# Kernel optimization log

Hardware: AMD Instinct MI355X
Metric: run time of the kernel (lower is better)

The kernel has to match this reference:

```python
import jax, jax.numpy as jnp
import numpy as np

B, S, HQ, HKV, DH = 1, 2048, 32, 8, 128
DE = HQ * DH  # DEmbed = 4096
G = HQ // HKV  # GQA group size = 4


def apply_rope(x, cs):
    # x: [B, S, H, DH]; cs: [2, S, 1, DH//2] (broadcast over B via leading dims)
    d = x.shape[-1] // 2
    x1, x2 = x[..., :d], x[..., d:]
    y1 = x1 * cs[0] + x2 * cs[1]
    y2 = -x1 * cs[1] + x2 * cs[0]
    return jnp.concatenate([y1, y2], axis=-1)


def setup_inputs() -> dict:
    key = jax.random.key(0)
    ks = jax.random.split(key, 5)
    x = jax.random.normal(ks[0], (B, S, DE), dtype=jnp.float32)
    # Precomputed rotary tables, shaped [2, S, 1, DH//2] so they broadcast over [B,S,H,DH//2]
    half = DH // 2
    inv_freq = 1.0 / (10000.0 ** (np.arange(half, dtype=np.float64) / half))
    ang = np.arange(S, dtype=np.float64)[:, None] * inv_freq[None, :]
    cos_sin_RoPE = jnp.asarray(
        np.stack([np.cos(ang), np.sin(ang)])[:, :, None, :], dtype=jnp.float32
    )
    sc = DE ** -0.5
    wq = jax.random.normal(ks[1], (DE, HQ * DH), dtype=jnp.float32) * sc
    wk = jax.random.normal(ks[2], (DE, HKV * DH), dtype=jnp.float32) * sc
    wv = jax.random.normal(ks[3], (DE, HKV * DH), dtype=jnp.float32) * sc
    wo = jax.random.normal(ks[4], (DE, DE), dtype=jnp.float32) * sc
    return {"x": x, "cos_sin_RoPE": cos_sin_RoPE, "wq": wq, "wk": wk, "wv": wv, "wo": wo}


def reference(x, cos_sin_RoPE, wq, wk, wv, wo):
    b, s, _ = x.shape
    q = (x @ wq).reshape(b, s, HQ, DH)
    k = (x @ wk).reshape(b, s, HKV, DH)
    v = (x @ wv).reshape(b, s, HKV, DH)
    q = apply_rope(q, cos_sin_RoPE)
    k = apply_rope(k, cos_sin_RoPE)
    # GQA causal SDPA: group query heads per kv head
    q = q.transpose(0, 2, 1, 3).reshape(b, HKV, G, s, DH)  # [b,kv,g,s,d]
    k = k.transpose(0, 2, 1, 3)  # [b,kv,s,d]
    v = v.transpose(0, 2, 1, 3)  # [b,kv,s,d]
    scale = DH ** -0.5
    scores = jnp.einsum('bkgsd,bktd->bkgst', q, k) * scale  # [b,kv,g,s,s]
    mask = jnp.tril(jnp.ones((s, s), dtype=bool))
    scores = jnp.where(mask, scores, jnp.finfo(scores.dtype).min)
    p = jax.nn.softmax(scores, axis=-1)
    o = jnp.einsum('bkgst,bktd->bkgsd', p, v)  # [b,kv,g,s,d]
    o = o.transpose(0, 3, 1, 2, 4).reshape(b, s, HQ * DH)
    return o @ wo
```

## Files before the change

### kernel.cpp

```cpp
#include <hip/hip_runtime.h>
#include <hip/hip_bf16.h>
#include <cstdint>
#include <cstddef>

typedef __bf16 bf16x8 __attribute__((ext_vector_type(8)));
typedef float floatx4 __attribute__((ext_vector_type(4)));

#define MFMA(a, b, c) __builtin_amdgcn_mfma_f32_16x16x32_bf16((a), (b), (c), 0, 0, 0)

__device__ __forceinline__ unsigned short f2bf(float f) {
  unsigned u = __builtin_bit_cast(unsigned, f);
  u += 0x7fffu + ((u >> 16) & 1u);
  return (unsigned short)(u >> 16);
}
__device__ __forceinline__ float bf2f(unsigned short h) {
  unsigned u = ((unsigned)h) << 16;
  return __builtin_bit_cast(float, u);
}
__device__ __forceinline__ float fast_exp2(float x) {
#if __has_builtin(__builtin_amdgcn_exp2f)
  return __builtin_amdgcn_exp2f(x);
#else
  return exp2f(x);
#endif
}

__device__ __forceinline__ void gl2lds16(const unsigned short* g, unsigned short* l) {
  __builtin_amdgcn_global_load_lds(
      (const __attribute__((address_space(1))) unsigned int*)g,
      (__attribute__((address_space(3))) unsigned int*)l, 16, 0, 0);
}

__global__ void convert_f32_bf16(const float* __restrict__ src,
                                 unsigned short* __restrict__ dst, int n4) {
  int i = blockIdx.x * 256 + threadIdx.x;
  if (i >= n4) return;
  float4 f = ((const float4*)src)[i];
  ushort4 o;
  o.x = f2bf(f.x); o.y = f2bf(f.y); o.z = f2bf(f.z); o.w = f2bf(f.w);
  ((ushort4*)dst)[i] = o;
}

__global__ void transpose_f32_bf16(const float* __restrict__ src,
                                   unsigned short* __restrict__ dst, int K, int N) {
  __shared__ float tile[64 * 65];
  int tn = blockIdx.x * 64, tk = blockIdx.y * 64;
  int r = threadIdx.x >> 4;
  int c4 = (threadIdx.x & 15) * 4;
#pragma unroll
  for (int i = 0; i < 4; i++) {
    float4 f = *(const float4*)&src[(size_t)(tk + r + 16 * i) * N + tn + c4];
    float* tr = &tile[(r + 16 * i) * 65 + c4];
    tr[0] = f.x; tr[1] = f.y; tr[2] = f.z; tr[3] = f.w;
  }
  __syncthreads();
#pragma unroll
  for (int i = 0; i < 4; i++) {
    ushort4 o;
    o.x = f2bf(tile[(c4 + 0) * 65 + r + 16 * i]);
    o.y = f2bf(tile[(c4 + 1) * 65 + r + 16 * i]);
    o.z = f2bf(tile[(c4 + 2) * 65 + r + 16 * i]);
    o.w = f2bf(tile[(c4 + 3) * 65 + r + 16 * i]);
    *(ushort4*)&dst[(size_t)(tn + r + 16 * i) * K + tk + c4] = o;
  }
}

template <bool F32OUT>
__global__ __launch_bounds__(256) void gemm_bt(const unsigned short* __restrict__ A,
                        const unsigned short* __restrict__ Bt,
                        void* __restrict__ C, int M, int N, int K) {
  __shared__ alignas(16) unsigned short Alds[128 * 64];
  __shared__ alignas(16) unsigned short Blds[128 * 64];
  const int tid = threadIdx.x;
  const int w = tid >> 6, L = tid & 63;
  const int lr = L & 15, lg = L >> 4;
  const int bm = blockIdx.y * 128, bn = blockIdx.x * 128;
  const int wm = (w >> 1) * 64, wn = (w & 1) * 64;
  floatx4 acc[4][4] = {};

  const int srow = L >> 3;
  const int pcg = L & 7;
  const int scg = (pcg ^ srow) * 8;

  const unsigned short* Ag = &A[(size_t)(bm + w * 32 + srow) * K + scg];
  const unsigned short* Bg = &Bt[(size_t)(bn + w * 32 + srow) * K + scg];
  unsigned short* Al = &Alds[(w * 32 + srow) * 64 + pcg * 8];
  unsigned short* Bl = &Blds[(w * 32 + srow) * 64 + pcg * 8];

  for (int k0 = 0; k0 < K; k0 += 64) {
#pragma unroll
    for (int i = 0; i < 4; i++) {
      gl2lds16(Ag + (size_t)(i * 8) * K, Al + i * 8 * 64);
      gl2lds16(Bg + (size_t)(i * 8) * K, Bl + i * 8 * 64);
    }
    Ag += 64; Bg += 64;
    __syncthreads();

#pragma unroll
    for (int kk = 0; kk < 2; kk++) {
      const int ofs = ((kk * 4 + lg) ^ (lr & 7)) * 8;
      bf16x8 af[4], bfr[4];
#pragma unroll
      for (int i = 0; i < 4; i++) {
        af[i]  = *(const bf16x8*)&Alds[(wm + i * 16 + lr) * 64 + ofs];
        bfr[i] = *(const bf16x8*)&Blds[(wn + i * 16 + lr) * 64 + ofs];
      }
#pragma unroll
      for (int mi = 0; mi < 4; mi++)
#pragma unroll
        for (int ni = 0; ni < 4; ni++)
          acc[mi][ni] = MFMA(af[mi], bfr[ni], acc[mi][ni]);
    }
    __syncthreads();
  }

#pragma unroll
  for (int mi = 0; mi < 4; mi++) {
#pragma unroll
    for (int ni = 0; ni < 4; ni++) {
#pragma unroll
      for (int r = 0; r < 4; r++) {
        size_t row = bm + wm + mi * 16 + lg * 4 + r;
        size_t col = bn + wn + ni * 16 + lr;
        float v = acc[mi][ni][r];
        if constexpr (F32OUT) ((float*)C)[row * N + col] = v;
        else ((unsigned short*)C)[row * N + col] = f2bf(v);
      }
    }
  }
}

__global__ void rope_kernel(unsigned short* __restrict__ X, const float* __restrict__ cs,
                            int H, int rowStride, int colOff, float scale) {
  int idx = blockIdx.x * 256 + threadIdx.x;
  int d = idx & 63;
  int h = (idx >> 6) % H;
  int s = idx / (64 * H);
  size_t base = (size_t)s * rowStride + colOff + (size_t)h * 128;
  float x1 = bf2f(X[base + d]), x2 = bf2f(X[base + d + 64]);
  float c = cs[s * 64 + d];
  float sn = cs[2048 * 64 + s * 64 + d];
  float y1 = (x1 * c + x2 * sn) * scale;
  float y2 = (x2 * c - x1 * sn) * scale;
  X[base + d] = f2bf(y1);
  X[base + d + 64] = f2bf(y2);
}

__global__ void v_transpose(const unsigned short* __restrict__ QKV,
                            unsigned short* __restrict__ Vt) {
  __shared__ unsigned short tile[32][33];
  int h = blockIdx.z;
  int s0 = blockIdx.x * 32, d0 = blockIdx.y * 32;
  int c = threadIdx.x & 31, r0 = threadIdx.x >> 5;
#pragma unroll
  for (int i = 0; i < 32; i += 8)
    tile[r0 + i][c] = QKV[(size_t)(s0 + r0 + i) * 6144 + 5120 + h * 128 + d0 + c];
  __syncthreads();
#pragma unroll
  for (int i = 0; i < 32; i += 8)
    Vt[(size_t)(h * 128 + d0 + r0 + i) * 2048 + s0 + c] = tile[c][r0 + i];
}

__global__ __launch_bounds__(256) void flash_kernel(
    const unsigned short* __restrict__ QKV,
    const unsigned short* __restrict__ Vt,
    unsigned short* __restrict__ O) {
  constexpr int PSTR = 72;
  __shared__ alignas(16) unsigned short Klds[64 * 128];
  __shared__ alignas(16) unsigned short Vlds[128 * 64];
  __shared__ alignas(16) unsigned short Plds[4 * 32 * PSTR];
  const int tid = threadIdx.x, w = tid >> 6, L = tid & 63;
  const int lr = L & 15, lg = L >> 4;
  const int bid = blockIdx.x;
  const int hk = bid & 7;
  const int hp = (bid >> 3) & 1;
  const int qb = 31 - (bid >> 4);
  const int hq = hk * 4 + hp * 2 + (w & 1);
  const int qr0 = qb * 64 + (w >> 1) * 32;
  const unsigned short* Kg = QKV + 4096;

  const int k_row = tid >> 4, k_lcg = tid & 15;
  const unsigned short* KgT = &Kg[(size_t)k_row * 6144 + hk * 128 + ((k_lcg ^ (k_row & 15)) * 8)];
  unsigned short* KlT = &Klds[k_row * 128 + k_lcg * 8];
  const int v_row = tid >> 3, v_lcg = tid & 7;
  const unsigned short* VgT = &Vt[(size_t)(hk * 128 + v_row) * 2048 + ((v_lcg ^ (v_row & 7)) * 8)];
  unsigned short* VlT = &Vlds[v_row * 64 + v_lcg * 8];

  bf16x8 qf[2][4];
#pragma unroll
  for (int mi = 0; mi < 2; mi++)
#pragma unroll
    for (int c = 0; c < 4; c++)
      qf[mi][c] = *(const bf16x8*)&QKV[(size_t)(qr0 + mi * 16 + lr) * 6144 + hq * 128 + c * 32 + lg * 8];

  floatx4 oacc[2][8] = {};
  float l_lane[2][4] = {};
  unsigned short* pw = &Plds[w * 32 * PSTR];

  for (int t = 0; t <= qb; t++) {
    const int kv0 = t * 64;
    __syncthreads();
#pragma unroll
    for (int i = 0; i < 4; i++) {
      gl2lds16(KgT + (size_t)(kv0 + i * 16) * 6144, KlT + i * 16 * 128);
      gl2lds16(VgT + kv0 + (size_t)(i * 32) * 2048, VlT + i * 32 * 64);
    }
    __syncthreads();

#pragma unroll
    for (int nt = 0; nt < 4; nt++) {
      bf16x8 kf[4];
#pragma unroll
      for (int c = 0; c < 4; c++)
        kf[c] = *(const bf16x8*)&Klds[(nt * 16 + lr) * 128 + (((c * 4 + lg) ^ lr) * 8)];
      floatx4 sc[2];
#pragma unroll
      for (int mi = 0; mi < 2; mi++) {
        floatx4 a = {};
#pragma unroll
        for (int c = 0; c < 4; c++) a = MFMA(qf[mi][c], kf[c], a);
        sc[mi] = a;
      }
      if (t == qb) {
#pragma unroll
        for (int mi = 0; mi < 2; mi++)
#pragma unroll
          for (int r = 0; r < 4; r++)
            if (kv0 + nt * 16 + lr > qr0 + mi * 16 + lg * 4 + r) sc[mi][r] = -3e38f;
      }
#pragma unroll
      for (int mi = 0; mi < 2; mi++)
#pragma unroll
        for (int r = 0; r < 4; r++) {
          float p = fast_exp2(sc[mi][r]);
          l_lane[mi][r] += p;
          pw[(mi * 16 + lg * 4 + r) * PSTR + nt * 16 + lr] = f2bf(p);
        }
    }

    bf16x8 pf[2][2];
#pragma unroll
    for (int mi = 0; mi < 2; mi++)
#pragma unroll
      for (int c = 0; c < 2; c++)
        pf[mi][c] = *(const bf16x8*)&pw[(mi * 16 + lr) * PSTR + c * 32 + lg * 8];

#pragma unroll
    for (int n = 0; n < 8; n++) {
#pragma unroll
      for (int c = 0; c < 2; c++) {
        bf16x8 vf = *(const bf16x8*)&Vlds[(n * 16 + lr) * 64 + (((c * 4 + lg) ^ (lr & 7)) * 8)];
#pragma unroll
        for (int mi = 0; mi < 2; mi++) oacc[mi][n] = MFMA(pf[mi][c], vf, oacc[mi][n]);
      }
    }
  }

  float linv[2][4];
#pragma unroll
  for (int mi = 0; mi < 2; mi++)
#pragma unroll
    for (int r = 0; r < 4; r++) {
      float l = l_lane[mi][r];
      l += __shfl_xor(l, 1);
      l += __shfl_xor(l, 2);
      l += __shfl_xor(l, 4);
      l += __shfl_xor(l, 8);
      linv[mi][r] = 1.0f / l;
    }

#pragma unroll
  for (int mi = 0; mi < 2; mi++)
#pragma unroll
    for (int n = 0; n < 8; n++)
#pragma unroll
      for (int r = 0; r < 4; r++) {
        size_t row = qr0 + mi * 16 + lg * 4 + r;
        size_t col = (size_t)hq * 128 + n * 16 + lr;
        O[row * 4096 + col] = f2bf(oacc[mi][n][r] * linv[mi][r]);
      }
}

extern "C" void kernel_launch(void* const* d_in, const int* in_sizes, int n_in,
                              void* d_out, int out_size, void* d_ws, size_t ws_size,
                              hipStream_t stream) {
  const float* x  = (const float*)d_in[0];
  const float* cs = (const float*)d_in[1];
  const float* wq = (const float*)d_in[2];
  const float* wk = (const float*)d_in[3];
  const float* wv = (const float*)d_in[4];
  const float* wo = (const float*)d_in[5];
  float* out = (float*)d_out;

  char* ws = (char*)d_ws;
  unsigned short* xb   = (unsigned short*)(ws);
  unsigned short* wqt  = (unsigned short*)(ws + 16777216);
  unsigned short* wkt  = (unsigned short*)(ws + 50331648);
  unsigned short* wvt  = (unsigned short*)(ws + 58720256);
  unsigned short* wot  = (unsigned short*)(ws + 67108864);
  unsigned short* QKVb = (unsigned short*)(ws + 100663296);
  unsigned short* Vtb  = (unsigned short*)(ws + 125829120);
  unsigned short* Ob   = xb;

  convert_f32_bf16<<<8192, 256, 0, stream>>>(x, xb, 2097152);
  transpose_f32_bf16<<<dim3(64, 64), 256, 0, stream>>>(wq, wqt, 4096, 4096);
  transpose_f32_bf16<<<dim3(16, 64), 256, 0, stream>>>(wk, wkt, 4096, 1024);
  transpose_f32_bf16<<<dim3(16, 64), 256, 0, stream>>>(wv, wvt, 4096, 1024);
  transpose_f32_bf16<<<dim3(64, 64), 256, 0, stream>>>(wo, wot, 4096, 4096);

  gemm_bt<false><<<dim3(48, 16), 256, 0, stream>>>(xb, wqt, QKVb, 2048, 6144, 4096);

  rope_kernel<<<16384, 256, 0, stream>>>(QKVb, cs, 32, 6144, 0, 0.12751743f);
  rope_kernel<<<4096, 256, 0, stream>>>(QKVb, cs, 8, 6144, 4096, 1.0f);

  v_transpose<<<dim3(64, 4, 8), 256, 0, stream>>>(QKVb, Vtb);

  flash_kernel<<<512, 256, 0, stream>>>(QKVb, Vtb, Ob);

  gemm_bt<true><<<dim3(32, 16), 256, 0, stream>>>(Ob, wot, out, 2048, 4096, 4096);
}
```

Before: 501.5 us.

## Replace GEMM with double-buffered 512-thread pipelined kernel and vectorize RoPE

Replaces the single-buffered 128x128 GEMM with a 512-thread kernel using 256-wide N tiles (256x256 for QKV, 128x256 for output projection). It double-buffers LDS, interleaves global-to-LDS prefetches of tile T+2 between MFMA clusters, and uses explicit waitcnt, barriers and setprio to overlap memory with compute. RoPE is also vectorized to process four elements per thread with 64-bit loads and stores. The output-projection grid shrinks to 256 blocks, and the larger tiles raise register and LDS pressure, which could hurt occupancy or load balance.

```diff
diff --git a/kernel.cpp b/kernel.cpp
--- a/kernel.cpp
+++ b/kernel.cpp
@@ -7,6 +7,10 @@
 typedef float floatx4 __attribute__((ext_vector_type(4)));
 
 #define MFMA(a, b, c) __builtin_amdgcn_mfma_f32_16x16x32_bf16((a), (b), (c), 0, 0, 0)
+#define WAITVM(N) asm volatile("s_waitcnt vmcnt(" #N ")" ::: "memory")
+#define WAITLGKM0() asm volatile("s_waitcnt lgkmcnt(0)" ::: "memory")
+#define BARRIER() do { asm volatile("" ::: "memory"); __builtin_amdgcn_s_barrier(); asm volatile("" ::: "memory"); } while (0)
+#define SCHEDBAR() __builtin_amdgcn_sched_barrier(0)
 
 __device__ __forceinline__ unsigned short f2bf(float f) {
   unsigned u = __builtin_bit_cast(unsigned, f);
@@ -65,61 +69,128 @@
   }
 }
 
-template <bool F32OUT>
-__global__ __launch_bounds__(256) void gemm_bt(const unsigned short* __restrict__ A,
-                        const unsigned short* __restrict__ Bt,
-                        void* __restrict__ C, int M, int N, int K) {
-  __shared__ alignas(16) unsigned short Alds[128 * 64];
-  __shared__ alignas(16) unsigned short Blds[128 * 64];
+template <int MI, int MLO>
+__device__ __forceinline__ void mfma_cluster(floatx4 (&acc)[MI][4],
+                                             const bf16x8* a, const bf16x8* b) {
+  __builtin_amdgcn_s_setprio(1);
+#pragma unroll
+  for (int mi = 0; mi < 4; ++mi)
+#pragma unroll
+    for (int ni = 0; ni < 4; ++ni)
+      acc[MLO + mi][ni] = MFMA(a[MLO + mi], b[ni], acc[MLO + mi][ni]);
+  __builtin_amdgcn_s_setprio(0);
+}
+
+template <int MI, bool F32OUT>
+__global__ __launch_bounds__(512, 2) void gemm_pipe(
+    const unsigned short* __restrict__ A,
+    const unsigned short* __restrict__ Bt,
+    void* __restrict__ C, int M, int N, int K) {
+  constexpr int BM = MI * 32;
+  constexpr int NSA = BM / 64;
+  __shared__ alignas(16) unsigned short Al[2][BM * 64];
+  __shared__ alignas(16) unsigned short Bl[2][256 * 64];
   const int tid = threadIdx.x;
   const int w = tid >> 6, L = tid & 63;
   const int lr = L & 15, lg = L >> 4;
-  const int bm = blockIdx.y * 128, bn = blockIdx.x * 128;
-  const int wm = (w >> 1) * 64, wn = (w & 1) * 64;
-  floatx4 acc[4][4] = {};
-
-  const int srow = L >> 3;
-  const int pcg = L & 7;
-  const int scg = (pcg ^ srow) * 8;
-
-  const unsigned short* Ag = &A[(size_t)(bm + w * 32 + srow) * K + scg];
-  const unsigned short* Bg = &Bt[(size_t)(bn + w * 32 + srow) * K + scg];
-  unsigned short* Al = &Alds[(w * 32 + srow) * 64 + pcg * 8];
-  unsigned short* Bl = &Blds[(w * 32 + srow) * 64 + pcg * 8];
-
-  for (int k0 = 0; k0 < K; k0 += 64) {
-#pragma unroll
-    for (int i = 0; i < 4; i++) {
-      gl2lds16(Ag + (size_t)(i * 8) * K, Al + i * 8 * 64);
-      gl2lds16(Bg + (size_t)(i * 8) * K, Bl + i * 8 * 64);
-    }
-    Ag += 64; Bg += 64;
-    __syncthreads();
-
-#pragma unroll
-    for (int kk = 0; kk < 2; kk++) {
-      const int ofs = ((kk * 4 + lg) ^ (lr & 7)) * 8;
-      bf16x8 af[4], bfr[4];
-#pragma unroll
-      for (int i = 0; i < 4; i++) {
-        af[i]  = *(const bf16x8*)&Alds[(wm + i * 16 + lr) * 64 + ofs];
-        bfr[i] = *(const bf16x8*)&Blds[(wn + i * 16 + lr) * 64 + ofs];
-      }
-#pragma unroll
-      for (int mi = 0; mi < 4; mi++)
-#pragma unroll
-        for (int ni = 0; ni < 4; ni++)
-          acc[mi][ni] = MFMA(af[mi], bfr[ni], acc[mi][ni]);
-    }
-    __syncthreads();
-  }
-
-#pragma unroll
-  for (int mi = 0; mi < 4; mi++) {
-#pragma unroll
-    for (int ni = 0; ni < 4; ni++) {
-#pragma unroll
-      for (int r = 0; r < 4; r++) {
+  const int bm = blockIdx.y * BM, bn = blockIdx.x * 256;
+  const int wm = (w >> 2) * (MI * 16);
+  const int wn = (w & 3) * 64;
+  const int NT = K >> 6;
+
+  const int srow = tid >> 3, spcg = tid & 7;
+  const unsigned short* Ag = &A[(size_t)(bm + srow) * K + ((spcg ^ (srow & 7)) * 8)];
+  const unsigned short* Bg = &Bt[(size_t)(bn + srow) * K + ((spcg ^ (srow & 7)) * 8)];
+  unsigned short* AlT = &Al[0][0] + tid * 8;
+  unsigned short* BlT = &Bl[0][0] + tid * 8;
+
+#pragma unroll
+  for (int t = 0; t < 2; ++t) {
+#pragma unroll
+    for (int j = 0; j < NSA; ++j)
+      gl2lds16(Ag + (size_t)(j * 64) * K + t * 64, AlT + t * (BM * 64) + j * 4096);
+#pragma unroll
+    for (int j = 0; j < 4; ++j)
+      gl2lds16(Bg + (size_t)(j * 64) * K + t * 64, BlT + t * (256 * 64) + j * 4096);
+  }
+
+  floatx4 acc[MI][4] = {};
+
+  if constexpr (MI == 8) WAITVM(8); else WAITVM(6);
+  BARRIER();
+
+  for (int T = 0; T < NT; ++T) {
+    const int b = T & 1;
+    const unsigned short* Ab = &Al[b][0];
+    const unsigned short* Bb = &Bl[b][0];
+    bf16x8 a0[MI], a1[MI], b0[4], b1[4];
+#pragma unroll
+    for (int mi = 0; mi < MI; ++mi)
+      a0[mi] = *(const bf16x8*)&Ab[(wm + mi * 16 + lr) * 64 + ((lg ^ (lr & 7)) * 8)];
+#pragma unroll
+    for (int ni = 0; ni < 4; ++ni)
+      b0[ni] = *(const bf16x8*)&Bb[(wn + ni * 16 + lr) * 64 + ((lg ^ (lr & 7)) * 8)];
+#pragma unroll
+    for (int mi = 0; mi < MI; ++mi)
+      a1[mi] = *(const bf16x8*)&Ab[(wm + mi * 16 + lr) * 64 + (((4 + lg) ^ (lr & 7)) * 8)];
+#pragma unroll
+    for (int ni = 0; ni < 4; ++ni)
+      b1[ni] = *(const bf16x8*)&Bb[(wn + ni * 16 + lr) * 64 + (((4 + lg) ^ (lr & 7)) * 8)];
+
+    const bool st = (T + 2) < NT;
+    const size_t kofs = (size_t)(T + 2) * 64;
+    unsigned short* Ad = AlT + b * (BM * 64);
+    unsigned short* Bd = BlT + b * (256 * 64);
+
+    if constexpr (MI == 8) {
+      mfma_cluster<8, 0>(acc, a0, b0);
+      WAITLGKM0();
+      BARRIER(); SCHEDBAR();
+      if (st) {
+        gl2lds16(Ag + kofs, Ad);
+        gl2lds16(Ag + (size_t)64 * K + kofs, Ad + 4096);
+        gl2lds16(Ag + (size_t)128 * K + kofs, Ad + 8192);
+      }
+      mfma_cluster<8, 4>(acc, a0, b0);
+      BARRIER(); SCHEDBAR();
+      if (st) {
+        gl2lds16(Ag + (size_t)192 * K + kofs, Ad + 12288);
+        gl2lds16(Bg + kofs, Bd);
+        gl2lds16(Bg + (size_t)64 * K + kofs, Bd + 4096);
+      }
+      mfma_cluster<8, 0>(acc, a1, b1);
+      BARRIER(); SCHEDBAR();
+      if (st) {
+        gl2lds16(Bg + (size_t)128 * K + kofs, Bd + 8192);
+        gl2lds16(Bg + (size_t)192 * K + kofs, Bd + 12288);
+      }
+      mfma_cluster<8, 4>(acc, a1, b1);
+      if (st) { WAITVM(8); } else if (T + 1 < NT) { WAITVM(0); }
+      BARRIER(); SCHEDBAR();
+    } else {
+      mfma_cluster<4, 0>(acc, a0, b0);
+      WAITLGKM0();
+      BARRIER(); SCHEDBAR();
+      if (st) {
+        gl2lds16(Ag + kofs, Ad);
+        gl2lds16(Ag + (size_t)64 * K + kofs, Ad + 4096);
+        gl2lds16(Bg + kofs, Bd);
+        gl2lds16(Bg + (size_t)64 * K + kofs, Bd + 4096);
+        gl2lds16(Bg + (size_t)128 * K + kofs, Bd + 8192);
+        gl2lds16(Bg + (size_t)192 * K + kofs, Bd + 12288);
+      }
+      mfma_cluster<4, 0>(acc, a1, b1);
+      if (st) { WAITVM(6); } else if (T + 1 < NT) { WAITVM(0); }
+      BARRIER(); SCHEDBAR();
+    }
+  }
+
+#pragma unroll
+  for (int mi = 0; mi < MI; ++mi) {
+#pragma unroll
+    for (int ni = 0; ni < 4; ++ni) {
+#pragma unroll
+      for (int r = 0; r < 4; ++r) {
         size_t row = bm + wm + mi * 16 + lg * 4 + r;
         size_t col = bn + wn + ni * 16 + lr;
         float v = acc[mi][ni][r];
@@ -133,17 +204,37 @@
 __global__ void rope_kernel(unsigned short* __restrict__ X, const float* __restrict__ cs,
                             int H, int rowStride, int colOff, float scale) {
   int idx = blockIdx.x * 256 + threadIdx.x;
-  int d = idx & 63;
-  int h = (idx >> 6) % H;
-  int s = idx / (64 * H);
-  size_t base = (size_t)s * rowStride + colOff + (size_t)h * 128;
-  float x1 = bf2f(X[base + d]), x2 = bf2f(X[base + d + 64]);
-  float c = cs[s * 64 + d];
-  float sn = cs[2048 * 64 + s * 64 + d];
-  float y1 = (x1 * c + x2 * sn) * scale;
-  float y2 = (x2 * c - x1 * sn) * scale;
-  X[base + d] = f2bf(y1);
-  X[base + d + 64] = f2bf(y2);
+  int dg = idx & 15;
+  int h = (idx >> 4) % H;
+  int s = idx / (16 * H);
+  size_t base = (size_t)s * rowStride + colOff + (size_t)h * 128 + dg * 4;
+  ushort4 xa = *(const ushort4*)&X[base];
+  ushort4 xb = *(const ushort4*)&X[base + 64];
+  float4 c = *(const float4*)&cs[s * 64 + dg * 4];
+  float4 sn = *(const float4*)&cs[2048 * 64 + s * 64 + dg * 4];
+  ushort4 oa, ob;
+  {
+    float x1 = bf2f(xa.x), x2 = bf2f(xb.x);
+    oa.x = f2bf((x1 * c.x + x2 * sn.x) * scale);
+    ob.x = f2bf((x2 * c.x - x1 * sn.x) * scale);
+  }
+  {
+    float x1 = bf2f(xa.y), x2 = bf2f(xb.y);
+    oa.y = f2bf((x1 * c.y + x2 * sn.y) * scale);
+    ob.y = f2bf((x2 * c.y - x1 * sn.y) * scale);
+  }
+  {
+    float x1 = bf2f(xa.z), x2 = bf2f(xb.z);
+    oa.z = f2bf((x1 * c.z + x2 * sn.z) * scale);
+    ob.z = f2bf((x2 * c.z - x1 * sn.z) * scale);
+  }
+  {
+    float x1 = bf2f(xa.w), x2 = bf2f(xb.w);
+    oa.w = f2bf((x1 * c.w + x2 * sn.w) * scale);
+    ob.w = f2bf((x2 * c.w - x1 * sn.w) * scale);
+  }
+  *(ushort4*)&X[base] = oa;
+  *(ushort4*)&X[base + 64] = ob;
 }
 
 __global__ void v_transpose(const unsigned short* __restrict__ QKV,
@@ -308,14 +399,14 @@
   transpose_f32_bf16<<<dim3(16, 64), 256, 0, stream>>>(wv, wvt, 4096, 1024);
   transpose_f32_bf16<<<dim3(64, 64), 256, 0, stream>>>(wo, wot, 4096, 4096);
 
-  gemm_bt<false><<<dim3(48, 16), 256, 0, stream>>>(xb, wqt, QKVb, 2048, 6144, 4096);
-
-  rope_kernel<<<16384, 256, 0, stream>>>(QKVb, cs, 32, 6144, 0, 0.12751743f);
-  rope_kernel<<<4096, 256, 0, stream>>>(QKVb, cs, 8, 6144, 4096, 1.0f);
+  gemm_pipe<8, false><<<dim3(24, 8), 512, 0, stream>>>(xb, wqt, QKVb, 2048, 6144, 4096);
+
+  rope_kernel<<<4096, 256, 0, stream>>>(QKVb, cs, 32, 6144, 0, 0.12751743f);
+  rope_kernel<<<1024, 256, 0, stream>>>(QKVb, cs, 8, 6144, 4096, 1.0f);
 
   v_transpose<<<dim3(64, 4, 8), 256, 0, stream>>>(QKVb, Vtb);
 
   flash_kernel<<<512, 256, 0, stream>>>(QKVb, Vtb, Ob);
 
-  gemm_bt<true><<<dim3(32, 16), 256, 0, stream>>>(Ob, wot, out, 2048, 4096, 4096);
-}
+  gemm_pipe<4, true><<<dim3(16, 16), 512, 0, stream>>>(Ob, wot, out, 2048, 4096, 4096);
+}
```

Result: no change. 495.2 us (-1.2%).

## Double-buffer LDS tiles in GEMM and flash attention, vectorize RoPE

Applied to the files above, without the earlier changes.

The GEMM now keeps two LDS stages and prefetches the next K tile with async global-to-LDS loads while MFMAs run on the current one. It uses explicit vmcnt waits and raw barriers in place of __syncthreads, and sets launch bounds for two blocks per CU. The flash kernel double-buffers the K tile and issues the next K load after the score phase so it overlaps the PV MFMAs. RoPE processes four elements per thread with vector loads to cut launch and memory-instruction overhead. Doubling LDS may lower occupancy, and the hand-placed waitcnt values must match the load counts exactly.

```diff
diff --git a/kernel.cpp b/kernel.cpp
--- a/kernel.cpp
+++ b/kernel.cpp
@@ -7,6 +7,8 @@
 typedef float floatx4 __attribute__((ext_vector_type(4)));
 
 #define MFMA(a, b, c) __builtin_amdgcn_mfma_f32_16x16x32_bf16((a), (b), (c), 0, 0, 0)
+#define WAITVM(N) asm volatile("s_waitcnt vmcnt(" #N ")" ::: "memory")
+#define BARRIER() do { asm volatile("" ::: "memory"); __builtin_amdgcn_s_barrier(); asm volatile("" ::: "memory"); } while (0)
 
 __device__ __forceinline__ unsigned short f2bf(float f) {
   unsigned u = __builtin_bit_cast(unsigned, f);
@@ -66,44 +68,59 @@
 }
 
 template <bool F32OUT>
-__global__ __launch_bounds__(256) void gemm_bt(const unsigned short* __restrict__ A,
-                        const unsigned short* __restrict__ Bt,
-                        void* __restrict__ C, int M, int N, int K) {
-  __shared__ alignas(16) unsigned short Alds[128 * 64];
-  __shared__ alignas(16) unsigned short Blds[128 * 64];
+__global__ __launch_bounds__(256, 2) void gemm2p(
+    const unsigned short* __restrict__ A,
+    const unsigned short* __restrict__ Bt,
+    void* __restrict__ C, int M, int N, int K) {
+  __shared__ alignas(16) unsigned short Al[2 * 128 * 64];
+  __shared__ alignas(16) unsigned short Bl[2 * 128 * 64];
   const int tid = threadIdx.x;
   const int w = tid >> 6, L = tid & 63;
-  const int lr = L & 15, lg = L >> 4;
+  const int lr = L & 15, lg = L >> 4, lr7 = lr & 7;
   const int bm = blockIdx.y * 128, bn = blockIdx.x * 128;
   const int wm = (w >> 1) * 64, wn = (w & 1) * 64;
+  const int NT = K >> 6;
+
+  const int srow = tid >> 3, scg = tid & 7;
+  const unsigned short* Ag = &A[(size_t)(bm + srow) * K + ((scg ^ (srow & 7)) * 8)];
+  const unsigned short* Bg = &Bt[(size_t)(bn + srow) * K + ((scg ^ (srow & 7)) * 8)];
+  unsigned short* AlT = Al + tid * 8;
+  unsigned short* BlT = Bl + tid * 8;
+
+#pragma unroll
+  for (int c = 0; c < 4; c++) {
+    gl2lds16(Ag + (size_t)(c * 32) * K, AlT + c * 2048);
+    gl2lds16(Bg + (size_t)(c * 32) * K, BlT + c * 2048);
+  }
+
   floatx4 acc[4][4] = {};
 
-  const int srow = L >> 3;
-  const int pcg = L & 7;
-  const int scg = (pcg ^ srow) * 8;
-
-  const unsigned short* Ag = &A[(size_t)(bm + w * 32 + srow) * K + scg];
-  const unsigned short* Bg = &Bt[(size_t)(bn + w * 32 + srow) * K + scg];
-  unsigned short* Al = &Alds[(w * 32 + srow) * 64 + pcg * 8];
-  unsigned short* Bl = &Blds[(w * 32 + srow) * 64 + pcg * 8];
-
-  for (int k0 = 0; k0 < K; k0 += 64) {
-#pragma unroll
-    for (int i = 0; i < 4; i++) {
-      gl2lds16(Ag + (size_t)(i * 8) * K, Al + i * 8 * 64);
-      gl2lds16(Bg + (size_t)(i * 8) * K, Bl + i * 8 * 64);
-    }
-    Ag += 64; Bg += 64;
-    __syncthreads();
-
+  for (int T = 0; T < NT; ++T) {
+    const int buf = T & 1;
+    if (T + 1 < NT) {
+      const size_t kofs = (size_t)(T + 1) * 64;
+      unsigned short* Ad = AlT + (buf ^ 1) * 8192;
+      unsigned short* Bd = BlT + (buf ^ 1) * 8192;
+#pragma unroll
+      for (int c = 0; c < 4; c++) {
+        gl2lds16(Ag + (size_t)(c * 32) * K + kofs, Ad + c * 2048);
+        gl2lds16(Bg + (size_t)(c * 32) * K + kofs, Bd + c * 2048);
+      }
+      WAITVM(8);
+    } else {
+      WAITVM(0);
+    }
+    BARRIER();
+
+    const unsigned short* Ab = Al + buf * 8192;
+    const unsigned short* Bb = Bl + buf * 8192;
 #pragma unroll
     for (int kk = 0; kk < 2; kk++) {
-      const int ofs = ((kk * 4 + lg) ^ (lr & 7)) * 8;
       bf16x8 af[4], bfr[4];
 #pragma unroll
       for (int i = 0; i < 4; i++) {
-        af[i]  = *(const bf16x8*)&Alds[(wm + i * 16 + lr) * 64 + ofs];
-        bfr[i] = *(const bf16x8*)&Blds[(wn + i * 16 + lr) * 64 + ofs];
+        af[i]  = *(const bf16x8*)&Ab[(wm + i * 16 + lr) * 64 + (((kk * 4 + lg) ^ lr7) * 8)];
+        bfr[i] = *(const bf16x8*)&Bb[(wn + i * 16 + lr) * 64 + (((kk * 4 + lg) ^ lr7) * 8)];
       }
 #pragma unroll
       for (int mi = 0; mi < 4; mi++)
@@ -111,7 +128,7 @@
         for (int ni = 0; ni < 4; ni++)
           acc[mi][ni] = MFMA(af[mi], bfr[ni], acc[mi][ni]);
     }
-    __syncthreads();
+    BARRIER();
   }
 
 #pragma unroll
@@ -133,17 +150,37 @@
 __global__ void rope_kernel(unsigned short* __restrict__ X, const float* __restrict__ cs,
                             int H, int rowStride, int colOff, float scale) {
   int idx = blockIdx.x * 256 + threadIdx.x;
-  int d = idx & 63;
-  int h = (idx >> 6) % H;
-  int s = idx / (64 * H);
-  size_t base = (size_t)s * rowStride + colOff + (size_t)h * 128;
-  float x1 = bf2f(X[base + d]), x2 = bf2f(X[base + d + 64]);
-  float c = cs[s * 64 + d];
-  float sn = cs[2048 * 64 + s * 64 + d];
-  float y1 = (x1 * c + x2 * sn) * scale;
-  float y2 = (x2 * c - x1 * sn) * scale;
-  X[base + d] = f2bf(y1);
-  X[base + d + 64] = f2bf(y2);
+  int dg = idx & 15;
+  int h = (idx >> 4) % H;
+  int s = idx / (16 * H);
+  size_t base = (size_t)s * rowStride + colOff + (size_t)h * 128 + dg * 4;
+  ushort4 xa = *(const ushort4*)&X[base];
+  ushort4 xb = *(const ushort4*)&X[base + 64];
+  float4 c = *(const float4*)&cs[s * 64 + dg * 4];
+  float4 sn = *(const float4*)&cs[2048 * 64 + s * 64 + dg * 4];
+  ushort4 oa, ob;
+  {
+    float x1 = bf2f(xa.x), x2 = bf2f(xb.x);
+    oa.x = f2bf((x1 * c.x + x2 * sn.x) * scale);
+    ob.x = f2bf((x2 * c.x - x1 * sn.x) * scale);
+  }
+  {
+    float x1 = bf2f(xa.y), x2 = bf2f(xb.y);
+    oa.y = f2bf((x1 * c.y + x2 * sn.y) * scale);
+    ob.y = f2bf((x2 * c.y - x1 * sn.y) * scale);
+  }
+  {
+    float x1 = bf2f(xa.z), x2 = bf2f(xb.z);
+    oa.z = f2bf((x1 * c.z + x2 * sn.z) * scale);
+    ob.z = f2bf((x2 * c.z - x1 * sn.z) * scale);
+  }
+  {
+    float x1 = bf2f(xa.w), x2 = bf2f(xb.w);
+    oa.w = f2bf((x1 * c.w + x2 * sn.w) * scale);
+    ob.w = f2bf((x2 * c.w - x1 * sn.w) * scale);
+  }
+  *(ushort4*)&X[base] = oa;
+  *(ushort4*)&X[base + 64] = ob;
 }
 
 __global__ void v_transpose(const unsigned short* __restrict__ QKV,
@@ -166,7 +203,7 @@
     const unsigned short* __restrict__ Vt,
     unsigned short* __restrict__ O) {
   constexpr int PSTR = 72;
-  __shared__ alignas(16) unsigned short Klds[64 * 128];
+  __shared__ alignas(16) unsigned short Klds[2 * 64 * 128];
   __shared__ alignas(16) unsigned short Vlds[128 * 64];
   __shared__ alignas(16) unsigned short Plds[4 * 32 * PSTR];
   const int tid = threadIdx.x, w = tid >> 6, L = tid & 63;
@@ -186,6 +223,10 @@
   const unsigned short* VgT = &Vt[(size_t)(hk * 128 + v_row) * 2048 + ((v_lcg ^ (v_row & 7)) * 8)];
   unsigned short* VlT = &Vlds[v_row * 64 + v_lcg * 8];
 
+#pragma unroll
+  for (int i = 0; i < 4; i++)
+    gl2lds16(KgT + (size_t)(i * 16) * 6144, KlT + i * 16 * 128);
+
   bf16x8 qf[2][4];
 #pragma unroll
   for (int mi = 0; mi < 2; mi++)
@@ -199,20 +240,20 @@
 
   for (int t = 0; t <= qb; t++) {
     const int kv0 = t * 64;
-    __syncthreads();
-#pragma unroll
-    for (int i = 0; i < 4; i++) {
-      gl2lds16(KgT + (size_t)(kv0 + i * 16) * 6144, KlT + i * 16 * 128);
+    const int kb = t & 1;
+    WAITVM(0);
+    BARRIER();
+#pragma unroll
+    for (int i = 0; i < 4; i++)
       gl2lds16(VgT + kv0 + (size_t)(i * 32) * 2048, VlT + i * 32 * 64);
-    }
-    __syncthreads();
-
+
+    const unsigned short* Kl = &Klds[kb * (64 * 128)];
 #pragma unroll
     for (int nt = 0; nt < 4; nt++) {
       bf16x8 kf[4];
 #pragma unroll
       for (int c = 0; c < 4; c++)
-        kf[c] = *(const bf16x8*)&Klds[(nt * 16 + lr) * 128 + (((c * 4 + lg) ^ lr) * 8)];
+        kf[c] = *(const bf16x8*)&Kl[(nt * 16 + lr) * 128 + (((c * 4 + lg) ^ lr) * 8)];
       floatx4 sc[2];
 #pragma unroll
       for (int mi = 0; mi < 2; mi++) {
@@ -237,6 +278,17 @@
           pw[(mi * 16 + lg * 4 + r) * PSTR + nt * 16 + lr] = f2bf(p);
         }
     }
+
+    if (t < qb) {
+      unsigned short* Kd = KlT + (kb ^ 1) * (64 * 128);
+#pragma unroll
+      for (int i = 0; i < 4; i++)
+        gl2lds16(KgT + (size_t)(kv0 + 64 + i * 16) * 6144, Kd + i * 16 * 128);
+      WAITVM(4);
+    } else {
+      WAITVM(0);
+    }
+    BARRIER();
 
     bf16x8 pf[2][2];
 #pragma unroll
@@ -308,14 +360,14 @@
   transpose_f32_bf16<<<dim3(16, 64), 256, 0, stream>>>(wv, wvt, 4096, 1024);
   transpose_f32_bf16<<<dim3(64, 64), 256, 0, stream>>>(wo, wot, 4096, 4096);
 
-  gemm_bt<false><<<dim3(48, 16), 256, 0, stream>>>(xb, wqt, QKVb, 2048, 6144, 4096);
-
-  rope_kernel<<<16384, 256, 0, stream>>>(QKVb, cs, 32, 6144, 0, 0.12751743f);
-  rope_kernel<<<4096, 256, 0, stream>>>(QKVb, cs, 8, 6144, 4096, 1.0f);
+  gemm2p<false><<<dim3(48, 16), 256, 0, stream>>>(xb, wqt, QKVb, 2048, 6144, 4096);
+
+  rope_kernel<<<4096, 256, 0, stream>>>(QKVb, cs, 32, 6144, 0, 0.12751743f);
+  rope_kernel<<<1024, 256, 0, stream>>>(QKVb, cs, 8, 6144, 4096, 1.0f);
 
   v_transpose<<<dim3(64, 4, 8), 256, 0, stream>>>(QKVb, Vtb);
 
   flash_kernel<<<512, 256, 0, stream>>>(QKVb, Vtb, Ob);
 
-  gemm_bt<true><<<dim3(32, 16), 256, 0, stream>>>(Ob, wot, out, 2048, 4096, 4096);
-}
+  gemm2p<true><<<dim3(32, 16), 256, 0, stream>>>(Ob, wot, out, 2048, 4096, 4096);
+}
```

After: 528.3 us. 1.05x slower.
